# Optimization experiments

Hardware: AMD Instinct MI355X
Metric: run time of the kernel (lower is better)

Reference implementation:

```python
import jax, jax.numpy as jnp
import numpy as np

N = 100000        # number of nodes
E = 3200000       # number of edges (avg degree 32)
D_IN = 128
D_OUT = 128


def setup_inputs() -> dict:
    key = jax.random.key(0)
    k_x, k_src, k_dst, k_w, k_W, k_b = jax.random.split(key, 6)
    x = jax.random.normal(k_x, (N, D_IN), dtype=jnp.float32)
    edge_src = jax.random.randint(k_src, (E,), 0, N, dtype=jnp.int32)
    edge_dst = jnp.sort(jax.random.randint(k_dst, (E,), 0, N, dtype=jnp.int32))
    edge_weight = jax.random.uniform(k_w, (E,), dtype=jnp.float32)
    # Linear params, init uniform(-stdv, stdv) with stdv = 1/sqrt(in_features)
    stdv = 1.0 / np.sqrt(D_IN)
    W = jax.random.uniform(k_W, (D_IN, D_OUT), dtype=jnp.float32, minval=-stdv, maxval=stdv)
    b = jax.random.uniform(k_b, (D_OUT,), dtype=jnp.float32, minval=-stdv, maxval=stdv)
    return {"x": x, "W": W, "b": b, "edge_weight": edge_weight,
            "edge_src": edge_src, "edge_dst": edge_dst}


def reference(x, W, b, edge_weight, edge_src, edge_dst):
    # support = W(input)  -- dense projection [N, D_OUT]
    support = x @ W + b
    # output = spmm(adj, support): out[dst] += w_e * support[src]
    msgs = support[edge_src] * edge_weight[:, None]          # [E, D_OUT]
    out = jax.ops.segment_sum(msgs, edge_dst, num_segments=x.shape[0])
    return out
```

## Files before the change

### kernel.cpp

```cpp
#include <hip/hip_runtime.h>

#define D 128

typedef unsigned short u16;
typedef __attribute__((ext_vector_type(8))) short bf16x8;
typedef __attribute__((ext_vector_type(4))) float f32x4;

__device__ __forceinline__ u16 f32_to_bf16(float f) {
    unsigned u = __float_as_uint(f);
    unsigned rounding = 0x7fffu + ((u >> 16) & 1u);
    return (u16)((u + rounding) >> 16);
}

__device__ __forceinline__ float bf16_to_f32(u16 s) {
    return __uint_as_float(((unsigned)s) << 16);
}

__global__ __launch_bounds__(256) void prep_kernel(
    const float* __restrict__ W, u16* __restrict__ Wt)
{
    #pragma unroll 4
    for (int i = 0; i < 64; ++i) {
        int idx = i * 256 + threadIdx.x;
        int n = idx >> 7;
        int k = idx & 127;
        Wt[idx] = f32_to_bf16(W[k * 128 + n]);
    }
}

__global__ __launch_bounds__(256) void gemm_mfma_kernel(
    const float* __restrict__ x, const u16* __restrict__ Wt,
    const float* __restrict__ b, u16* __restrict__ sup, int N)
{
    const int lane = threadIdx.x & 63;
    const int wave = threadIdx.x >> 6;
    const int col  = lane & 15;
    const int quad = lane >> 4;
    const int row0 = blockIdx.x * 64 + wave * 16;
    const int m    = row0 + col;
    const bool mvalid = (m < N);

    f32x4 acc[8];
    #pragma unroll
    for (int nt = 0; nt < 8; ++nt) {
        float bias = b[nt * 16 + col];
        acc[nt][0] = bias; acc[nt][1] = bias;
        acc[nt][2] = bias; acc[nt][3] = bias;
    }

    const float* xrow = x + (size_t)m * D;

    #pragma unroll
    for (int ks = 0; ks < 4; ++ks) {
        const int k0 = ks * 32 + quad * 8;

        float af[8];
        if (mvalid) {
            float4 v0 = *(const float4*)(xrow + k0);
            float4 v1 = *(const float4*)(xrow + k0 + 4);
            af[0] = v0.x; af[1] = v0.y; af[2] = v0.z; af[3] = v0.w;
            af[4] = v1.x; af[5] = v1.y; af[6] = v1.z; af[7] = v1.w;
        } else {
            #pragma unroll
            for (int j = 0; j < 8; ++j) af[j] = 0.f;
        }

        bf16x8 ahi, alo;
        #pragma unroll
        for (int j = 0; j < 8; ++j) {
            u16 h = f32_to_bf16(af[j]);
            float r = af[j] - bf16_to_f32(h);
            ahi[j] = (short)h;
            alo[j] = (short)f32_to_bf16(r);
        }

        #pragma unroll
        for (int nt = 0; nt < 8; ++nt) {
            bf16x8 bfrag = *(const bf16x8*)(Wt + (size_t)(nt * 16 + col) * D + k0);
            acc[nt] = __builtin_amdgcn_mfma_f32_16x16x32_bf16(alo, bfrag, acc[nt], 0, 0, 0);
            acc[nt] = __builtin_amdgcn_mfma_f32_16x16x32_bf16(ahi, bfrag, acc[nt], 0, 0, 0);
        }
    }

    #pragma unroll
    for (int reg = 0; reg < 4; ++reg) {
        int r = row0 + quad * 4 + reg;
        if (r < N) {
            #pragma unroll
            for (int nt = 0; nt < 8; ++nt) {
                sup[(size_t)r * D + nt * 16 + col] = f32_to_bf16(acc[nt][reg]);
            }
        }
    }
}

__global__ __launch_bounds__(256) void rowptr_kernel(
    const int* __restrict__ edst, int* __restrict__ rp, int E, int N)
{
    int e = blockIdx.x * 256 + threadIdx.x;
    if (e >= E) return;
    int d = edst[e];
    int prev = (e == 0) ? -1 : edst[e - 1];
    for (int n = prev + 1; n <= d; ++n) rp[n] = e;
    if (e == E - 1) {
        for (int n = d + 1; n <= N; ++n) rp[n] = E;
    }
}

__global__ __launch_bounds__(256) void spmm_kernel(
    const u16* __restrict__ sup, const float* __restrict__ ew,
    const int* __restrict__ esrc, const int* __restrict__ rp,
    float* __restrict__ out, int N)
{
    const int wid  = (blockIdx.x * 256 + threadIdx.x) >> 6;
    const int lane = threadIdx.x & 63;
    if (wid >= N) return;

    const int start = rp[wid];
    const int end   = rp[wid + 1];
    const unsigned off = lane * 2;

    float acc0 = 0.f, acc1 = 0.f, acc2 = 0.f, acc3 = 0.f;

    for (int base = start; base < end; base += 64) {
        int cnt = end - base;
        if (cnt > 64) cnt = 64;
        int cnt8 = (cnt + 7) & ~7;

        int mi = base + lane;
        int   sv = (mi < end) ? esrc[mi] : 0;
        float wv = (mi < end) ? ew[mi]   : 0.f;

        for (int i = 0; i < cnt8; i += 8) {
            int   s0 = __shfl(sv, i    ), s1 = __shfl(sv, i + 1);
            int   s2 = __shfl(sv, i + 2), s3 = __shfl(sv, i + 3);
            int   s4 = __shfl(sv, i + 4), s5 = __shfl(sv, i + 5);
            int   s6 = __shfl(sv, i + 6), s7 = __shfl(sv, i + 7);
            float w0 = __shfl(wv, i    ), w1 = __shfl(wv, i + 1);
            float w2 = __shfl(wv, i + 2), w3 = __shfl(wv, i + 3);
            float w4 = __shfl(wv, i + 4), w5 = __shfl(wv, i + 5);
            float w6 = __shfl(wv, i + 6), w7 = __shfl(wv, i + 7);

            unsigned u0 = *(const unsigned*)(sup + (size_t)s0 * D + off);
            unsigned u1 = *(const unsigned*)(sup + (size_t)s1 * D + off);
            unsigned u2 = *(const unsigned*)(sup + (size_t)s2 * D + off);
            unsigned u3 = *(const unsigned*)(sup + (size_t)s3 * D + off);
            unsigned u4 = *(const unsigned*)(sup + (size_t)s4 * D + off);
            unsigned u5 = *(const unsigned*)(sup + (size_t)s5 * D + off);
            unsigned u6 = *(const unsigned*)(sup + (size_t)s6 * D + off);
            unsigned u7 = *(const unsigned*)(sup + (size_t)s7 * D + off);

            acc0 = fmaf(w0, __uint_as_float(u0 << 16),          acc0);
            acc1 = fmaf(w0, __uint_as_float(u0 & 0xffff0000u),  acc1);
            acc2 = fmaf(w1, __uint_as_float(u1 << 16),          acc2);
            acc3 = fmaf(w1, __uint_as_float(u1 & 0xffff0000u),  acc3);
            acc0 = fmaf(w2, __uint_as_float(u2 << 16),          acc0);
            acc1 = fmaf(w2, __uint_as_float(u2 & 0xffff0000u),  acc1);
            acc2 = fmaf(w3, __uint_as_float(u3 << 16),          acc2);
            acc3 = fmaf(w3, __uint_as_float(u3 & 0xffff0000u),  acc3);
            acc0 = fmaf(w4, __uint_as_float(u4 << 16),          acc0);
            acc1 = fmaf(w4, __uint_as_float(u4 & 0xffff0000u),  acc1);
            acc2 = fmaf(w5, __uint_as_float(u5 << 16),          acc2);
            acc3 = fmaf(w5, __uint_as_float(u5 & 0xffff0000u),  acc3);
            acc0 = fmaf(w6, __uint_as_float(u6 << 16),          acc0);
            acc1 = fmaf(w6, __uint_as_float(u6 & 0xffff0000u),  acc1);
            acc2 = fmaf(w7, __uint_as_float(u7 << 16),          acc2);
            acc3 = fmaf(w7, __uint_as_float(u7 & 0xffff0000u),  acc3);
        }
    }

    float2 o;
    o.x = acc0 + acc2;
    o.y = acc1 + acc3;
    *(float2*)(out + (size_t)wid * D + lane * 2) = o;
}

extern "C" void kernel_launch(void* const* d_in, const int* in_sizes, int n_in,
                              void* d_out, int out_size, void* d_ws, size_t ws_size,
                              hipStream_t stream) {
    const float* x    = (const float*)d_in[0];
    const float* W    = (const float*)d_in[1];
    const float* b    = (const float*)d_in[2];
    const float* ew   = (const float*)d_in[3];
    const int*   esrc = (const int*)d_in[4];
    const int*   edst = (const int*)d_in[5];
    float* out = (float*)d_out;

    const int N = in_sizes[0] / D;
    const int E = in_sizes[3];

    u16* sup = (u16*)d_ws;
    int* rp  = (int*)((char*)d_ws + (size_t)N * D * sizeof(u16));
    u16* Wt  = (u16*)((char*)rp + ((size_t)N + 16) * sizeof(int));

    hipLaunchKernelGGL(prep_kernel, dim3(1), dim3(256), 0, stream, W, Wt);
    hipLaunchKernelGGL(gemm_mfma_kernel, dim3((N + 63) / 64), dim3(256), 0, stream,
                       x, Wt, b, sup, N);
    hipLaunchKernelGGL(rowptr_kernel, dim3((E + 255) / 256), dim3(256), 0, stream,
                       edst, rp, E, N);
    hipLaunchKernelGGL(spmm_kernel, dim3((N + 3) / 4), dim3(256), 0, stream,
                       sup, ew, esrc, rp, out, N);
}
```

Before: 275.7 us.

## Prefetch next edge batch indices in SpMM and parallelize weight transpose

The SpMM loop no longer loads 64 edge indices per wave and broadcasts them with shuffles. Each lane now loads the next 8 edge indices and weights directly, with uniform addresses, while the current 8 gathers are in flight, which software-pipelines the index fetch behind the row gathers. Row bounds are made wave-uniform with readfirstlane so they sit in scalar registers. The weight transpose kernel now runs on 64 blocks instead of one serial block. The new scheme issues redundant per-lane index loads that the shuffle approach avoided, and it pads tail edges with zero weights.

```diff
diff --git a/kernel.cpp b/kernel.cpp
--- a/kernel.cpp
+++ b/kernel.cpp
@@ -19,13 +19,10 @@
 __global__ __launch_bounds__(256) void prep_kernel(
     const float* __restrict__ W, u16* __restrict__ Wt)
 {
-    #pragma unroll 4
-    for (int i = 0; i < 64; ++i) {
-        int idx = i * 256 + threadIdx.x;
-        int n = idx >> 7;
-        int k = idx & 127;
-        Wt[idx] = f32_to_bf16(W[k * 128 + n]);
-    }
+    int idx = blockIdx.x * 256 + threadIdx.x;
+    int n = idx >> 7;
+    int k = idx & 127;
+    Wt[idx] = f32_to_bf16(W[k * 128 + n]);
 }
 
 __global__ __launch_bounds__(256) void gemm_mfma_kernel(
@@ -116,63 +113,66 @@
     const int lane = threadIdx.x & 63;
     if (wid >= N) return;
 
-    const int start = rp[wid];
-    const int end   = rp[wid + 1];
-    const unsigned off = lane * 2;
+    const int start = __builtin_amdgcn_readfirstlane(rp[wid]);
+    const int end   = __builtin_amdgcn_readfirstlane(rp[wid + 1]);
+    const unsigned off = (unsigned)lane * 2u;
 
     float acc0 = 0.f, acc1 = 0.f, acc2 = 0.f, acc3 = 0.f;
 
-    for (int base = start; base < end; base += 64) {
-        int cnt = end - base;
-        if (cnt > 64) cnt = 64;
-        int cnt8 = (cnt + 7) & ~7;
-
-        int mi = base + lane;
-        int   sv = (mi < end) ? esrc[mi] : 0;
-        float wv = (mi < end) ? ew[mi]   : 0.f;
-
-        for (int i = 0; i < cnt8; i += 8) {
-            int   s0 = __shfl(sv, i    ), s1 = __shfl(sv, i + 1);
-            int   s2 = __shfl(sv, i + 2), s3 = __shfl(sv, i + 3);
-            int   s4 = __shfl(sv, i + 4), s5 = __shfl(sv, i + 5);
-            int   s6 = __shfl(sv, i + 6), s7 = __shfl(sv, i + 7);
-            float w0 = __shfl(wv, i    ), w1 = __shfl(wv, i + 1);
-            float w2 = __shfl(wv, i + 2), w3 = __shfl(wv, i + 3);
-            float w4 = __shfl(wv, i + 4), w5 = __shfl(wv, i + 5);
-            float w6 = __shfl(wv, i + 6), w7 = __shfl(wv, i + 7);
-
-            unsigned u0 = *(const unsigned*)(sup + (size_t)s0 * D + off);
-            unsigned u1 = *(const unsigned*)(sup + (size_t)s1 * D + off);
-            unsigned u2 = *(const unsigned*)(sup + (size_t)s2 * D + off);
-            unsigned u3 = *(const unsigned*)(sup + (size_t)s3 * D + off);
-            unsigned u4 = *(const unsigned*)(sup + (size_t)s4 * D + off);
-            unsigned u5 = *(const unsigned*)(sup + (size_t)s5 * D + off);
-            unsigned u6 = *(const unsigned*)(sup + (size_t)s6 * D + off);
-            unsigned u7 = *(const unsigned*)(sup + (size_t)s7 * D + off);
-
-            acc0 = fmaf(w0, __uint_as_float(u0 << 16),          acc0);
-            acc1 = fmaf(w0, __uint_as_float(u0 & 0xffff0000u),  acc1);
-            acc2 = fmaf(w1, __uint_as_float(u1 << 16),          acc2);
-            acc3 = fmaf(w1, __uint_as_float(u1 & 0xffff0000u),  acc3);
-            acc0 = fmaf(w2, __uint_as_float(u2 << 16),          acc0);
-            acc1 = fmaf(w2, __uint_as_float(u2 & 0xffff0000u),  acc1);
-            acc2 = fmaf(w3, __uint_as_float(u3 << 16),          acc2);
-            acc3 = fmaf(w3, __uint_as_float(u3 & 0xffff0000u),  acc3);
-            acc0 = fmaf(w4, __uint_as_float(u4 << 16),          acc0);
-            acc1 = fmaf(w4, __uint_as_float(u4 & 0xffff0000u),  acc1);
-            acc2 = fmaf(w5, __uint_as_float(u5 << 16),          acc2);
-            acc3 = fmaf(w5, __uint_as_float(u5 & 0xffff0000u),  acc3);
-            acc0 = fmaf(w6, __uint_as_float(u6 << 16),          acc0);
-            acc1 = fmaf(w6, __uint_as_float(u6 & 0xffff0000u),  acc1);
-            acc2 = fmaf(w7, __uint_as_float(u7 << 16),          acc2);
-            acc3 = fmaf(w7, __uint_as_float(u7 & 0xffff0000u),  acc3);
+    int   sm[8];
+    float wm[8];
+
+    if (start < end) {
+        #pragma unroll
+        for (int k = 0; k < 8; ++k) {
+            int ik  = start + k;
+            int idx = (ik < end) ? ik : start;
+            sm[k] = esrc[idx];
+            wm[k] = (ik < end) ? ew[idx] : 0.f;
+        }
+    }
+
+    for (int e = start; e < end; e += 8) {
+        int   cs[8];
+        float cw[8];
+        #pragma unroll
+        for (int k = 0; k < 8; ++k) { cs[k] = sm[k]; cw[k] = wm[k]; }
+
+        unsigned u[8];
+        #pragma unroll
+        for (int k = 0; k < 8; ++k) {
+            u[k] = *(const unsigned*)(sup + (size_t)cs[k] * D + off);
+        }
+
+        int en = e + 8;
+        if (en < end) {
+            #pragma unroll
+            for (int k = 0; k < 8; ++k) {
+                int ik  = en + k;
+                int idx = (ik < end) ? ik : en;
+                sm[k] = esrc[idx];
+                wm[k] = (ik < end) ? ew[idx] : 0.f;
+            }
+        }
+
+        #pragma unroll
+        for (int k = 0; k < 8; ++k) {
+            float lo = __uint_as_float(u[k] << 16);
+            float hi = __uint_as_float(u[k] & 0xffff0000u);
+            if (k & 1) {
+                acc2 = fmaf(cw[k], lo, acc2);
+                acc3 = fmaf(cw[k], hi, acc3);
+            } else {
+                acc0 = fmaf(cw[k], lo, acc0);
+                acc1 = fmaf(cw[k], hi, acc1);
+            }
         }
     }
 
     float2 o;
     o.x = acc0 + acc2;
     o.y = acc1 + acc3;
-    *(float2*)(out + (size_t)wid * D + lane * 2) = o;
+    *(float2*)(out + (size_t)wid * D + off) = o;
 }
 
 extern "C" void kernel_launch(void* const* d_in, const int* in_sizes, int n_in,
@@ -193,7 +193,7 @@
     int* rp  = (int*)((char*)d_ws + (size_t)N * D * sizeof(u16));
     u16* Wt  = (u16*)((char*)rp + ((size_t)N + 16) * sizeof(int));
 
-    hipLaunchKernelGGL(prep_kernel, dim3(1), dim3(256), 0, stream, W, Wt);
+    hipLaunchKernelGGL(prep_kernel, dim3(64), dim3(256), 0, stream, W, Wt);
     hipLaunchKernelGGL(gemm_mfma_kernel, dim3((N + 63) / 64), dim3(256), 0, stream,
                        x, Wt, b, sup, N);
     hipLaunchKernelGGL(rowptr_kernel, dim3((E + 255) / 256), dim3(256), 0, stream,
```

Result: slower. 303.9 us (+10.2%).
